# Kernel tuning notes

Hardware: AMD Instinct MI355X
Metric: run time of the kernel (lower is better)

The kernel has to match this reference:

```python
import jax, jax.numpy as jnp
import numpy as np
from jax import lax

DN = ('NCHW', 'OIHW', 'NCHW')


def conv_s2(x, w, b):
    # Conv2d(kernel=4, stride=2, padding=1): halves H,W
    y = lax.conv_general_dilated(x, w, (2, 2), ((1, 1), (1, 1)), dimension_numbers=DN)
    return y + b[None, :, None, None]


def conv_1x1(x, w, b):
    y = lax.conv_general_dilated(x, w, (1, 1), ((0, 0), (0, 0)), dimension_numbers=DN)
    return y + b[None, :, None, None]


def convT_s2(x, w, b):
    # torch ConvTranspose2d(kernel=4, stride=2, padding=1); torch weight layout [I,O,kh,kw]
    wt = jnp.flip(w, (2, 3)).transpose(1, 0, 2, 3)  # -> [O,I,kh,kw], spatially flipped
    y = lax.conv_general_dilated(x, wt, (1, 1), ((2, 2), (2, 2)),
                                 lhs_dilation=(2, 2), dimension_numbers=DN)
    return y + b[None, :, None, None]


def setup_inputs() -> dict:
    key = jax.random.key(0)
    ks = jax.random.split(key, 20)
    f32 = jnp.float32
    s = 0.05  # small init scale to keep activations sane
    inp = {
        'x': jax.random.uniform(ks[0], (32, 3, 256, 256), dtype=f32),
        # encoder
        'ew1': jax.random.normal(ks[1], (128, 3, 4, 4), f32) * s,
        'eb1': jnp.zeros((128,), f32),
        'ew2': jax.random.normal(ks[2], (256, 128, 4, 4), f32) * s,
        'eb2': jnp.zeros((256,), f32),
        'ew3': jax.random.normal(ks[3], (512, 256, 4, 4), f32) * s,
        'eb3': jnp.zeros((512,), f32),
        # pre-VQ 1x1 conv
        'pw': jax.random.normal(ks[4], (64, 512, 1, 1), f32) * s,
        'pb': jnp.zeros((64,), f32),
        # codebook (torch.randn in module)
        'emb': jax.random.normal(ks[5], (512, 64), f32),
        # decoder (ConvTranspose2d weights: [in, out, kh, kw])
        'dw1': jax.random.normal(ks[6], (64, 256, 4, 4), f32) * s,
        'db1': jnp.zeros((256,), f32),
        'dw2': jax.random.normal(ks[7], (256, 128, 4, 4), f32) * s,
        'db2': jnp.zeros((128,), f32),
        'dw3': jax.random.normal(ks[8], (128, 3, 4, 4), f32) * s,
        'db3': jnp.zeros((3,), f32),
    }
    return inp


def reference(x, ew1, eb1, ew2, eb2, ew3, eb3, pw, pb, emb,
              dw1, db1, dw2, db2, dw3, db3):
    # encoder
    h = jax.nn.relu(conv_s2(x, ew1, eb1))
    h = jax.nn.relu(conv_s2(h, ew2, eb2))
    h = jax.nn.relu(conv_s2(h, ew3, eb3))
    z_e = conv_1x1(h, pw, pb)  # [B, D, H, W]

    b, d, hh, ww = z_e.shape
    x_flat = z_e.reshape(b, d, hh * ww).transpose(0, 2, 1)  # [B, HW, D]
    # squared distances via expansion (same math, no [B,HW,K,D] blowup)
    x2 = jnp.sum(x_flat ** 2, axis=-1, keepdims=True)        # [B, HW, 1]
    e2 = jnp.sum(emb ** 2, axis=-1)                          # [K]
    dist = x2 - 2.0 * jnp.einsum('bnd,kd->bnk', x_flat, emb) + e2[None, None, :]
    indices = jnp.argmin(dist, axis=2)                       # [B, HW]
    zq_flat = emb[indices]                                   # [B, HW, D]
    z_q = zq_flat.transpose(0, 2, 1).reshape(b, d, hh, ww)

    quant_loss = (jnp.mean((zq_flat - x_flat) ** 2) * 2.0)   # matches detach-symmetric mse in fwd value

    # decoder
    y = jax.nn.relu(convT_s2(z_q, dw1, db1))
    y = jax.nn.relu(convT_s2(y, dw2, db2))
    y = jax.nn.sigmoid(convT_s2(y, dw3, db3))
    return (y, quant_loss)
```

## Files before the change

### kernel.cpp

```cpp
#include <hip/hip_runtime.h>
#include <cstddef>
#include <cstdint>

typedef __attribute__((ext_vector_type(8))) _Float16 half8;
typedef __attribute__((ext_vector_type(4))) float f32x4;

static __device__ __forceinline__ unsigned packhl(float v) {
  _Float16 h = (_Float16)v;
  _Float16 l = (_Float16)((v - (float)h) * 2048.0f);
  return (unsigned)__builtin_bit_cast(unsigned short, h) |
         ((unsigned)__builtin_bit_cast(unsigned short, l) << 16);
}


template<int CIN>
__global__ __launch_bounds__(256) void wsplit_k(
    const float* __restrict__ W, _Float16* __restrict__ Wh,
    _Float16* __restrict__ Wl, int Cout) {
  constexpr int NCB = CIN / 32;
  int idx = blockIdx.x * 256 + threadIdx.x;
  if (idx >= Cout * CIN) return;
  int ci = idx % CIN, co = idx / CIN;
  int cb = ci >> 5, k8 = (ci >> 3) & 3, j = ci & 7;
  const float* wp = W + (size_t)idx * 16;
#pragma unroll
  for (int tap = 0; tap < 16; ++tap) {
    float w = wp[tap];
    _Float16 wh = (_Float16)w;
    _Float16 wl = (_Float16)((w - (float)wh) * 2048.0f);
    size_t o = (((size_t)(tap * NCB + cb) * 4 + k8) * Cout + co) * 8 + j;
    Wh[o] = wh; Wl[o] = wl;
  }
}

template<int CIN>
__global__ __launch_bounds__(256) void wsplitT_k(
    const float* __restrict__ W, _Float16* __restrict__ Wh,
    _Float16* __restrict__ Wl, int Cout) {
  constexpr int NCB = CIN / 32;
  int idx = blockIdx.x * 256 + threadIdx.x;
  if (idx >= CIN * Cout) return;
  int co = idx % Cout, ci = idx / Cout;
  int cb = ci >> 5, k8 = (ci >> 3) & 3, j = ci & 7;
  const float* wp = W + (size_t)idx * 16;
#pragma unroll
  for (int t = 0; t < 16; ++t) {
    int py = (t >> 3) & 1, px = (t >> 2) & 1, i0 = (t >> 1) & 1, i1 = t & 1;
    int kh = py ? (i0 ? 2 : 0) : (i0 ? 3 : 1);
    int kw = px ? (i1 ? 2 : 0) : (i1 ? 3 : 1);
    float w = wp[kh * 4 + kw];
    _Float16 wh = (_Float16)w;
    _Float16 wl = (_Float16)((w - (float)wh) * 2048.0f);
    size_t o = (((size_t)(t * NCB + cb) * 4 + k8) * Cout + co) * 8 + j;
    Wh[o] = wh; Wl[o] = wl;
  }
}

__global__ __launch_bounds__(256) void border_k(
    char* base, int c8n, int H2, int W2, size_t SAI, size_t LOFF, int nimg) {
  int nb = 2 * W2 + 2 * (H2 - 2);
  int tot = nimg * c8n * 2 * nb;
  int idx = blockIdx.x * 256 + threadIdx.x;
  if (idx >= tot) return;
  int s = idx % nb; int r = idx / nb;
  int pl = r & 1; r >>= 1;
  int c8 = r % c8n; int b = r / c8n;
  int y, x;
  if (s < W2)            { y = 0;       x = s; }
  else if (s < 2 * W2)   { y = H2 - 1;  x = s - W2; }
  else { int t = s - 2 * W2; y = 1 + (t >> 1); x = (t & 1) ? W2 - 1 : 0; }
  size_t PLANE = (size_t)H2 * W2 * 16;
  char* p = base + (size_t)b * SAI + (size_t)pl * LOFF + (size_t)c8 * PLANE
            + ((size_t)y * W2 + x) * 16;
  *(uint4*)p = make_uint4(0, 0, 0, 0);
}

template<int CIN, int COUT, int CGRP, int NF, int RELU, int PACKOUT, int SPLITIN>
__global__ __launch_bounds__(256) void conv_mfma2(
    const void* __restrict__ inP, const _Float16* __restrict__ Whg,
    const _Float16* __restrict__ Wlg, const float* __restrict__ bias,
    float* __restrict__ out, int Hin, int Win, size_t inSAI, size_t inLOFF) {
  constexpr int NCB  = CIN / 32;
  constexpr int MT   = COUT / CGRP;
  constexpr int MF   = MT / 64;
  constexpr int ROWS = 2 * NF + 2;
  constexpr int NPOS = ROWS * 34;
  constexpr int K8S  = NPOS + 6;
  const int Hout = Hin >> 1, Wout = Win >> 1;
  const int TW = Wout >> 4;
  __shared__ half8 Bh[4 * K8S], Bl[4 * K8S];
  const int tid = threadIdx.x;
  const int lane = tid & 63, w = tid >> 6;
  const int l15 = lane & 15, k8 = lane >> 4;
  unsigned nwg = gridDim.x * gridDim.y;
  unsigned id  = blockIdx.y * gridDim.x + blockIdx.x;
  unsigned sw  = (id & 7) * (nwg >> 3) + (id >> 3);
  const int bx = sw % gridDim.x, by = sw / gridDim.x;
  const int tx = bx % TW, ty = bx / TW;
  const int cg = by % CGRP;
  const int b  = by / CGRP;
  const int oy0 = ty * NF, ox0 = tx << 4;
  const int iy_org = 2 * oy0 - 1, ix_org = 2 * ox0 - 1;
  const int cbase = cg * MT + w * (MT / 4);
  const size_t HW = (size_t)Hin * Win;
  const size_t tapStride = (size_t)NCB * 4 * COUT * 8;

  unsigned goff[4];
  const char* baseh = nullptr;
  size_t PLANE = 0;
  if (SPLITIN) {
    const int W2 = Win + 2;
    PLANE = (size_t)(Hin + 2) * W2 * 16;
    constexpr int S0[4] = {0, 64, 128, NPOS - 64};
#pragma unroll
    for (int t = 0; t < 4; ++t) {
      int s = S0[t] + lane;
      int r = s / 17, c = s - r * 17;
      int hy = r >> 1, p = r & 1;
      int hx = (c << 1) | p;
      int iy = iy_org + hy + 1, ix = ix_org + hx + 1;
      goff[t] = (unsigned)(((size_t)iy * W2 + ix) * 16);
    }
    baseh = (const char*)inP + ((size_t)b * inSAI) + (size_t)w * PLANE;
  }

  f32x4 accM[MF][NF], accX[MF][NF];
#pragma unroll
  for (int m = 0; m < MF; ++m)
#pragma unroll
    for (int nf = 0; nf < NF; ++nf) {
      accM[m][nf] = f32x4{0,0,0,0};
      accX[m][nf] = f32x4{0,0,0,0};
    }

  for (int cb = 0; cb < NCB; ++cb) {
    __syncthreads();
    if (SPLITIN) {
      const char* pc = baseh + (size_t)cb * 4 * PLANE;
      char* lh = (char*)&Bh[w * K8S];
      char* ll = (char*)&Bl[w * K8S];
      constexpr int S0[4] = {0, 64, 128, NPOS - 64};
#pragma unroll
      for (int t = 0; t < 4; ++t) {
        __builtin_amdgcn_global_load_lds(
            (const __attribute__((address_space(1))) void*)(pc + goff[t]),
            (__attribute__((address_space(3))) void*)(lh + S0[t] * 16), 16, 0, 0);
        __builtin_amdgcn_global_load_lds(
            (const __attribute__((address_space(1))) void*)(pc + inLOFF + goff[t]),
            (__attribute__((address_space(3))) void*)(ll + S0[t] * 16), 16, 0, 0);
      }
    } else {
      const unsigned* inU = (const unsigned*)inP;
      for (int u = tid; u < NPOS * 4; u += 256) {
        int kk = u / NPOS, pos = u - kk * NPOS;
        int hy = pos / 34, hx = pos - hy * 34;
        int iy = iy_org + hy, ix = ix_org + hx;
        bool ok = (unsigned)iy < (unsigned)Hin && (unsigned)ix < (unsigned)Win;
        uint4 qa = {0,0,0,0}, qb = {0,0,0,0};
        if (ok) {
          const uint4* gp = (const uint4*)(inU +
              (((size_t)b * (CIN / 8) + cb * 4 + kk) * HW + (size_t)iy * Win + ix) * 8);
          qa = gp[0]; qb = gp[1];
        }
        unsigned av[8] = {qa.x, qa.y, qa.z, qa.w, qb.x, qb.y, qb.z, qb.w};
        half8 vh, vl;
#pragma unroll
        for (int j = 0; j < 8; ++j) {
          vh[j] = __builtin_bit_cast(_Float16, (unsigned short)(av[j] & 0xffffu));
          vl[j] = __builtin_bit_cast(_Float16, (unsigned short)(av[j] >> 16));
        }
        int slotBase = (hy * 2 + (hx & 1)) * 17 + (hx >> 1);
        Bh[kk * K8S + slotBase] = vh;
        Bl[kk * K8S + slotBase] = vl;
      }
    }
    __syncthreads();
    const _Float16* aph = Whg + (((size_t)cb * 4 + k8) * COUT + cbase + l15) * 8;
    const _Float16* apl = Wlg + (((size_t)cb * 4 + k8) * COUT + cbase + l15) * 8;
    half8 ah[2][MF], al[2][MF];
#pragma unroll
    for (int m = 0; m < MF; ++m) {
      ah[0][m] = *(const half8*)(aph + m * 128);
      al[0][m] = *(const half8*)(apl + m * 128);
    }
#pragma unroll
    for (int tp = 0; tp < 16; ++tp) {
      const int cur = tp & 1, nxt = cur ^ 1;
      if (tp < 15) {
#pragma unroll
        for (int m = 0; m < MF; ++m) {
          ah[nxt][m] = *(const half8*)(aph + (size_t)(tp + 1) * tapStride + m * 128);
          al[nxt][m] = *(const half8*)(apl + (size_t)(tp + 1) * tapStride + m * 128);
        }
      }
      const int kh = tp >> 2, kw = tp & 3;
      const int p = kw & 1, cidx = kw >> 1;
#pragma unroll
      for (int nf = 0; nf < NF; ++nf) {
        const int slot = k8 * K8S + ((2 * nf + kh) * 2 + p) * 17 + l15 + cidx;
        const half8 bh = Bh[slot], bl = Bl[slot];
#pragma unroll
        for (int m = 0; m < MF; ++m) {
          accM[m][nf] = __builtin_amdgcn_mfma_f32_16x16x32_f16(ah[cur][m], bh, accM[m][nf], 0, 0, 0);
          accX[m][nf] = __builtin_amdgcn_mfma_f32_16x16x32_f16(ah[cur][m], bl, accX[m][nf], 0, 0, 0);
          accX[m][nf] = __builtin_amdgcn_mfma_f32_16x16x32_f16(al[cur][m], bh, accX[m][nf], 0, 0, 0);
        }
      }
    }
  }
#pragma unroll
  for (int m = 0; m < MF; ++m)
#pragma unroll
    for (int nf = 0; nf < NF; ++nf) {
      int oy = oy0 + nf, ox = ox0 + l15;
      if (PACKOUT) {
        unsigned pk[4];
#pragma unroll
        for (int i = 0; i < 4; ++i) {
          int co = cbase + m * 16 + k8 * 4 + i;
          float v = accM[m][nf][i] + accX[m][nf][i] * (1.0f / 2048.0f) + bias[co];
          if (RELU) v = fmaxf(v, 0.0f);
          pk[i] = packhl(v);
        }
        int co8 = (cbase + m * 16 + k8 * 4) >> 3;
        int j0 = (k8 & 1) * 4;
        unsigned* outU = (unsigned*)out;
        *(uint4*)(outU + (((size_t)b * (COUT / 8) + co8) * ((size_t)Hout * Wout)
                          + (size_t)oy * Wout + ox) * 8 + j0) =
            make_uint4(pk[0], pk[1], pk[2], pk[3]);
      } else {
#pragma unroll
        for (int i = 0; i < 4; ++i) {
          int co = cbase + m * 16 + k8 * 4 + i;
          float v = accM[m][nf][i] + accX[m][nf][i] * (1.0f / 2048.0f) + bias[co];
          if (RELU) v = fmaxf(v, 0.0f);
          out[(((size_t)b * COUT + co) * Hout + oy) * Wout + ox] = v;
        }
      }
    }
}

template<int CIN, int RELU, int PACKIN, int PACKOUT>
__global__ __launch_bounds__(256) void convT_mfma(
    const float* __restrict__ in, const _Float16* __restrict__ Whg,
    const _Float16* __restrict__ Wlg, const float* __restrict__ bias,
    float* __restrict__ out, int Cout, int Hin, int Win) {
  constexpr int NCB = CIN / 32;
  const int Hout = Hin * 2, Wout = Win * 2;
  const int TW = Win >> 4;
  __shared__ half8 Bh[4 * 72], Bl[4 * 72];
  const int tid = threadIdx.x;
  const int lane = tid & 63, w = tid >> 6;
  const int l15 = lane & 15, k8 = lane >> 4;
  const int tx = blockIdx.x % TW, ty = blockIdx.x / TW;
  const int cbo = blockIdx.y % (Cout >> 6);
  const int b   = blockIdx.y / (Cout >> 6);
  const int ty0 = ty << 1, tx0 = tx << 4;
  const int co0 = (cbo << 6) + (w << 4);
  const size_t HW = (size_t)Hin * Win;
  const size_t tapStride = (size_t)NCB * 4 * Cout * 8;

  f32x4 accM[4][2], accX[4][2];
#pragma unroll
  for (int p = 0; p < 4; ++p)
#pragma unroll
    for (int nf = 0; nf < 2; ++nf) {
      accM[p][nf] = f32x4{0,0,0,0};
      accX[p][nf] = f32x4{0,0,0,0};
    }

  for (int cb = 0; cb < NCB; ++cb) {
    __syncthreads();
    for (int u = tid; u < 288; u += 256) {
      int pos = u % 72, kk = u / 72;
      int r = pos / 18, c = pos - r * 18;
      int iy = ty0 - 1 + r, ix = tx0 - 1 + c;
      bool ok = (unsigned)iy < (unsigned)Hin && (unsigned)ix < (unsigned)Win;
      half8 vh, vl;
      if (PACKIN) {
        uint4 qa = {0,0,0,0}, qb = {0,0,0,0};
        if (ok) {
          const uint4* gp = (const uint4*)((const unsigned*)in +
              (((size_t)b * (CIN / 8) + cb * 4 + kk) * HW + (size_t)iy * Win + ix) * 8);
          qa = gp[0]; qb = gp[1];
        }
        unsigned av[8] = {qa.x, qa.y, qa.z, qa.w, qb.x, qb.y, qb.z, qb.w};
#pragma unroll
        for (int j = 0; j < 8; ++j) {
          vh[j] = __builtin_bit_cast(_Float16, (unsigned short)(av[j] & 0xffffu));
          vl[j] = __builtin_bit_cast(_Float16, (unsigned short)(av[j] >> 16));
        }
      } else {
        const float* gp = in + ((size_t)b * CIN + cb * 32 + kk * 8) * HW
                          + (ptrdiff_t)iy * Win + ix;
#pragma unroll
        for (int j = 0; j < 8; ++j) {
          float x = ok ? gp[(size_t)j * HW] : 0.0f;
          _Float16 xh = (_Float16)x;
          vh[j] = xh; vl[j] = (_Float16)((x - (float)xh) * 2048.0f);
        }
      }
      Bh[kk * 72 + pos] = vh;
      Bl[kk * 72 + pos] = vl;
    }
    __syncthreads();
    const _Float16* aph = Whg + (((size_t)cb * 4 + k8) * Cout + co0 + l15) * 8;
    const _Float16* apl = Wlg + (((size_t)cb * 4 + k8) * Cout + co0 + l15) * 8;
    half8 ahA = *(const half8*)(aph);
    half8 alA = *(const half8*)(apl);
#pragma unroll
    for (int t = 0; t < 16; ++t) {
      half8 ahN, alN;
      if (t < 15) {
        ahN = *(const half8*)(aph + (size_t)(t + 1) * tapStride);
        alN = *(const half8*)(apl + (size_t)(t + 1) * tapStride);
      }
      const int py = (t >> 3) & 1, px = (t >> 2) & 1;
      const int i0 = (t >> 1) & 1, i1 = t & 1;
      const int dy = py ? (i0 ? 0 : 1) : (i0 ? -1 : 0);
      const int dx = px ? (i1 ? 0 : 1) : (i1 ? -1 : 0);
      const int p = py * 2 + px;
#pragma unroll
      for (int nf = 0; nf < 2; ++nf) {
        int slot = k8 * 72 + (nf + 1 + dy) * 18 + (l15 + 1 + dx);
        half8 bh = Bh[slot], bl = Bl[slot];
        accM[p][nf] = __builtin_amdgcn_mfma_f32_16x16x32_f16(ahA, bh, accM[p][nf], 0, 0, 0);
        accX[p][nf] = __builtin_amdgcn_mfma_f32_16x16x32_f16(ahA, bl, accX[p][nf], 0, 0, 0);
        accX[p][nf] = __builtin_amdgcn_mfma_f32_16x16x32_f16(alA, bh, accX[p][nf], 0, 0, 0);
      }
      if (t < 15) { ahA = ahN; alA = alN; }
    }
  }
#pragma unroll
  for (int nf = 0; nf < 2; ++nf) {
#pragma unroll
    for (int i = 0; i < 4; ++i) {
      int co = co0 + k8 * 4 + i;
      float bb = bias[co];
#pragma unroll
      for (int py = 0; py < 2; ++py) {
        float v0 = accM[py * 2 + 0][nf][i] + accX[py * 2 + 0][nf][i] * (1.0f / 2048.0f) + bb;
        float v1 = accM[py * 2 + 1][nf][i] + accX[py * 2 + 1][nf][i] * (1.0f / 2048.0f) + bb;
        if (RELU) { v0 = fmaxf(v0, 0.0f); v1 = fmaxf(v1, 0.0f); }
        int oy = 2 * (ty0 + nf) + py, ox = 2 * (tx0 + l15);
        if (PACKOUT) {
          unsigned* outU = (unsigned*)out;
          int co8 = (co0 >> 3) + (k8 >> 1);
          int j = (k8 * 4 + i) & 7;
          size_t base = ((size_t)b * (Cout / 8) + co8) * ((size_t)Hout * Wout);
          outU[(base + (size_t)oy * Wout + ox) * 8 + j]     = packhl(v0);
          outU[(base + (size_t)oy * Wout + ox + 1) * 8 + j] = packhl(v1);
        } else {
          *(float2*)(out + (((size_t)b * Cout + co) * Hout + oy) * Wout + ox) =
              make_float2(v0, v1);
        }
      }
    }
  }
}


template<int CIN, int G, int RELU, int PACKOUT>
__global__ __launch_bounds__(256) void conv_t(
    const float* __restrict__ in, const float* __restrict__ wt,
    const float* __restrict__ bias, float* __restrict__ out,
    int Cout, int Hin, int Win, size_t oSAI, size_t oLOFF) {
  const int Hout = Hin >> 1, Wout = Win >> 1;
  const int TW = Wout >> 4;
  __shared__ float tile[34 * 35];
  int tid = threadIdx.x;
  int oxl = tid & 15, oyl = tid >> 4;
  int tyt = blockIdx.x / TW, txt = blockIdx.x - tyt * TW;
  int oy0 = tyt << 4, ox0 = txt << 4;
  int cg = blockIdx.y % (Cout / G);
  int b  = blockIdx.y / (Cout / G);
  int co0 = cg * G;
  const int iy_org = 2 * oy0 - 1, ix_org = 2 * ox0 - 1;
  const float* ip = in + (size_t)b * CIN * Hin * Win;
  float acc[G];
#pragma unroll
  for (int j = 0; j < G; ++j) acc[j] = bias[co0 + j];
  const int lbase = (2 * oyl) * 35 + 2 * oxl;
  for (int ci = 0; ci < CIN; ++ci) {
    const float* ic = ip + (size_t)ci * Hin * Win;
    __syncthreads();
#pragma unroll
    for (int k = 0; k < 5; ++k) {
      int idx = tid + k * 256;
      if (idx < 34 * 34) {
        int r = idx / 34, c = idx - r * 34;
        int iy = iy_org + r, ix = ix_org + c;
        float v = ((unsigned)iy < (unsigned)Hin && (unsigned)ix < (unsigned)Win)
                      ? ic[(size_t)iy * Win + ix] : 0.0f;
        tile[r * 35 + c] = v;
      }
    }
    __syncthreads();
    float xv[16];
#pragma unroll
    for (int kh = 0; kh < 4; ++kh)
#pragma unroll
      for (int kw = 0; kw < 4; ++kw)
        xv[kh * 4 + kw] = tile[lbase + kh * 35 + kw];
    const float* wc = wt + ((size_t)co0 * CIN + ci) * 16;
#pragma unroll
    for (int j = 0; j < G; ++j) {
      const float* wj = wc + (size_t)j * CIN * 16;
#pragma unroll
      for (int t2 = 0; t2 < 16; ++t2) acc[j] = fmaf(xv[t2], wj[t2], acc[j]);
    }
  }
  int oy = oy0 + oyl, ox = ox0 + oxl;
  if (RELU) {
#pragma unroll
    for (int j = 0; j < G; ++j) acc[j] = fmaxf(acc[j], 0.0f);
  }
  if (PACKOUT == 2) {
    const int W2 = Wout + 2;
    const size_t PLANE = (size_t)(Hout + 2) * W2 * 16;
    char* ob0 = (char*)out + (size_t)b * oSAI
                + ((size_t)(oy + 1) * W2 + ox + 1) * 16;
#pragma unroll
    for (int mb = 0; mb < G / 8; ++mb) {
      half8 hv, lv;
#pragma unroll
      for (int j = 0; j < 8; ++j) {
        float v = acc[mb * 8 + j];
        _Float16 h = (_Float16)v;
        hv[j] = h; lv[j] = (_Float16)((v - (float)h) * 2048.0f);
      }
      char* ob = ob0 + (size_t)((co0 >> 3) + mb) * PLANE;
      *(half8*)ob = hv;
      *(half8*)(ob + oLOFF) = lv;
    }
  } else {
    size_t cs = (size_t)Hout * Wout;
    float* op = out + ((size_t)(b * Cout + co0) * Hout + oy) * Wout + ox;
#pragma unroll
    for (int j = 0; j < G; ++j) op[(size_t)j * cs] = acc[j];
  }
}

template<int CIN, int G>
__global__ __launch_bounds__(256) void conv1x1_k(
    const float* __restrict__ in, const float* __restrict__ wt,
    const float* __restrict__ bias, float* __restrict__ out,
    int Cout, int HW) {
  int hw = blockIdx.x * 256 + threadIdx.x;
  int cg = blockIdx.y % (Cout / G);
  int b  = blockIdx.y / (Cout / G);
  int co0 = cg * G;
  const float* ip = in + (size_t)b * CIN * HW + hw;
  float acc[G];
#pragma unroll
  for (int j = 0; j < G; ++j) acc[j] = bias[co0 + j];
#pragma unroll 4
  for (int ci = 0; ci < CIN; ++ci) {
    float xv = ip[(size_t)ci * HW];
#pragma unroll
    for (int j = 0; j < G; ++j)
      acc[j] = fmaf(xv, wt[(size_t)(co0 + j) * CIN + ci], acc[j]);
  }
  float* op = out + ((size_t)(b * Cout + co0)) * HW + hw;
#pragma unroll
  for (int j = 0; j < G; ++j) op[(size_t)j * HW] = acc[j];
}

__global__ __launch_bounds__(128) void vq_k(
    const float* __restrict__ ze, const float* __restrict__ emb,
    float* __restrict__ zq, float* __restrict__ partial) {
  __shared__ float4 se4[128 * 16];
  __shared__ float red[128];
  int tid = threadIdx.x;
  int gid = blockIdx.x * 128 + tid;
  int b = gid >> 10, n = gid & 1023;
  const float* zp = ze + ((size_t)b << 16) + n;
  float4 v4[16];
#pragma unroll
  for (int d = 0; d < 16; ++d) {
    v4[d].x = zp[(size_t)(4 * d + 0) << 10];
    v4[d].y = zp[(size_t)(4 * d + 1) << 10];
    v4[d].z = zp[(size_t)(4 * d + 2) << 10];
    v4[d].w = zp[(size_t)(4 * d + 3) << 10];
  }
  float best = 1e30f; int bi = 0;
  for (int c = 0; c < 4; ++c) {
    __syncthreads();
    for (int i = tid; i < 2048; i += 128)
      se4[i] = ((const float4*)emb)[(c << 11) + i];
    __syncthreads();
    for (int k = 0; k < 128; ++k) {
      const float4* e = se4 + (k << 4);
      float s = 0.0f;
#pragma unroll
      for (int d = 0; d < 16; ++d) {
        float4 ev = e[d];
        float t0 = v4[d].x - ev.x; s = fmaf(t0, t0, s);
        float t1 = v4[d].y - ev.y; s = fmaf(t1, t1, s);
        float t2 = v4[d].z - ev.z; s = fmaf(t2, t2, s);
        float t3 = v4[d].w - ev.w; s = fmaf(t3, t3, s);
      }
      if (s < best) { best = s; bi = (c << 7) + k; }
    }
  }
  const float4* eb4 = (const float4*)emb + ((size_t)bi << 4);
  float* qp = zq + ((size_t)b << 16) + n;
  float ls = 0.0f;
#pragma unroll
  for (int d = 0; d < 16; ++d) {
    float4 q = eb4[d];
    qp[(size_t)(4 * d + 0) << 10] = q.x;
    qp[(size_t)(4 * d + 1) << 10] = q.y;
    qp[(size_t)(4 * d + 2) << 10] = q.z;
    qp[(size_t)(4 * d + 3) << 10] = q.w;
    float t0 = q.x - v4[d].x; ls = fmaf(t0, t0, ls);
    float t1 = q.y - v4[d].y; ls = fmaf(t1, t1, ls);
    float t2 = q.z - v4[d].z; ls = fmaf(t2, t2, ls);
    float t3 = q.w - v4[d].w; ls = fmaf(t3, t3, ls);
  }
  red[tid] = ls;
  __syncthreads();
  for (int s = 64; s > 0; s >>= 1) {
    if (tid < s) red[tid] += red[tid + s];
    __syncthreads();
  }
  if (tid == 0) partial[blockIdx.x] = red[0];
}

__global__ __launch_bounds__(256) void loss_fin(
    const float* __restrict__ partial, float* __restrict__ out) {
  __shared__ float red[256];
  int t = threadIdx.x;
  red[t] = partial[t];
  __syncthreads();
  for (int s = 128; s > 0; s >>= 1) {
    if (t < s) red[t] += red[t + s];
    __syncthreads();
  }
  if (t == 0) out[0] = red[0] * (2.0f / 2097152.0f);
}

template<int CIN, int G, int ACT>
__global__ __launch_bounds__(256) void convT_t(
    const float* __restrict__ in, const float* __restrict__ wt,
    const float* __restrict__ bias, float* __restrict__ out,
    int Cout, int Hin, int Win) {
  const int Hout = Hin * 2, Wout = Win * 2;
  const int TW = Win >> 4;
  __shared__ float tile[18 * 19];
  int tid = threadIdx.x;
  int txl = tid & 15, tyl = tid >> 4;
  int tyt = blockIdx.x / TW, txt = blockIdx.x - tyt * TW;
  int ty0 = tyt << 4, tx0 = txt << 4;
  int og = blockIdx.y % (Cout / G);
  int b  = blockIdx.y / (Cout / G);
  int o0 = og * G;
  const int iy_org = ty0 - 1, ix_org = tx0 - 1;
  const float* ip = in + (size_t)b * CIN * Hin * Win;
  float a00[G], a01[G], a10[G], a11[G];
#pragma unroll
  for (int j = 0; j < G; ++j) {
    float bb = bias[o0 + j];
    a00[j] = bb; a01[j] = bb; a10[j] = bb; a11[j] = bb;
  }
  const int lb = tyl * 19 + txl;
  for (int i = 0; i < CIN; ++i) {
    const float* ic = ip + (size_t)i * Hin * Win;
    __syncthreads();
#pragma unroll
    for (int k = 0; k < 2; ++k) {
      int idx = tid + k * 256;
      if (idx < 18 * 18) {
        int r = idx / 18, c = idx - r * 18;
        int iy = iy_org + r, ix = ix_org + c;
        float v = ((unsigned)iy < (unsigned)Hin && (unsigned)ix < (unsigned)Win)
                      ? ic[(size_t)iy * Win + ix] : 0.0f;
        tile[r * 19 + c] = v;
      }
    }
    __syncthreads();
    float x00 = tile[lb],          x01 = tile[lb + 1],      x02 = tile[lb + 2];
    float x10 = tile[lb + 19],     x11 = tile[lb + 20],     x12 = tile[lb + 21];
    float x20 = tile[lb + 38],     x21 = tile[lb + 39],     x22 = tile[lb + 40];
    const float* wv = wt + ((size_t)i * Cout + o0) * 16;
#pragma unroll
    for (int j = 0; j < G; ++j) {
      const float* w4 = wv + j * 16;
      a00[j] = fmaf(x11, w4[5],  fmaf(x10, w4[7],  fmaf(x01, w4[13], fmaf(x00, w4[15], a00[j]))));
      a01[j] = fmaf(x12, w4[4],  fmaf(x11, w4[6],  fmaf(x02, w4[12], fmaf(x01, w4[14], a01[j]))));
      a10[j] = fmaf(x21, w4[1],  fmaf(x20, w4[3],  fmaf(x11, w4[9],  fmaf(x10, w4[11], a10[j]))));
      a11[j] = fmaf(x22, w4[0],  fmaf(x21, w4[2],  fmaf(x12, w4[8],  fmaf(x11, w4[10], a11[j]))));
    }
  }
  size_t cs = (size_t)Hout * Wout;
  int ty = ty0 + tyl, tx = tx0 + txl;
  size_t base = ((size_t)(b * Cout + o0) * Hout + 2 * (size_t)ty) * Wout + 2 * tx;
#pragma unroll
  for (int j = 0; j < G; ++j) {
    float v00 = a00[j], v01 = a01[j], v10 = a10[j], v11 = a11[j];
    if (ACT == 1) {
      v00 = fmaxf(v00, 0.0f); v01 = fmaxf(v01, 0.0f);
      v10 = fmaxf(v10, 0.0f); v11 = fmaxf(v11, 0.0f);
    } else if (ACT == 2) {
      v00 = 1.0f / (1.0f + expf(-v00)); v01 = 1.0f / (1.0f + expf(-v01));
      v10 = 1.0f / (1.0f + expf(-v10)); v11 = 1.0f / (1.0f + expf(-v11));
    }
    *(float2*)(out + base + (size_t)j * cs)        = make_float2(v00, v01);
    *(float2*)(out + base + (size_t)j * cs + Wout) = make_float2(v10, v11);
  }
}

extern "C" void kernel_launch(void* const* d_in, const int* in_sizes, int n_in,
                              void* d_out, int out_size, void* d_ws, size_t ws_size,
                              hipStream_t stream) {
  const float* x   = (const float*)d_in[0];
  const float* ew1 = (const float*)d_in[1];
  const float* eb1 = (const float*)d_in[2];
  const float* ew2 = (const float*)d_in[3];
  const float* eb2 = (const float*)d_in[4];
  const float* ew3 = (const float*)d_in[5];
  const float* eb3 = (const float*)d_in[6];
  const float* pw  = (const float*)d_in[7];
  const float* pb  = (const float*)d_in[8];
  const float* emb = (const float*)d_in[9];
  const float* dw1 = (const float*)d_in[10];
  const float* db1 = (const float*)d_in[11];
  const float* dw2 = (const float*)d_in[12];
  const float* db2 = (const float*)d_in[13];
  const float* dw3 = (const float*)d_in[14];
  const float* db3 = (const float*)d_in[15];
  float* out = (float*)d_out;
  char* ws = (char*)d_ws;

  const size_t H1PLANE = 130ull * 130ull * 16ull;
  const size_t H1LOFF  = 16ull * H1PLANE;
  const size_t SAI     = 2ull * H1LOFF;
  const size_t PER  = SAI + 4194304ull + 2ull * 262144ull;
  const size_t WEXT = 4096ull + 13631488ull;
  int CB = 32;
  while (CB > 1 && (size_t)CB * PER + WEXT > ws_size) CB >>= 1;
  const size_t SA = (size_t)CB * SAI;
  const size_t SB = (size_t)CB * 4194304ull;
  const size_t SC = (size_t)CB * 262144ull;
  float* A    = (float*)(ws);
  float* Bp   = (float*)(ws + SA);
  float* ze   = (float*)(ws + SA + SB);
  float* zq   = (float*)(ws + SA + SB + SC);
  float* part = (float*)(ws + SA + SB + 2 * SC);
  _Float16* wh2  = (_Float16*)(ws + SA + SB + 2 * SC + 4096);
  _Float16* wl2  = wh2 + 524288;
  _Float16* wh3  = wl2 + 524288;
  _Float16* wl3  = wh3 + 2097152;
  _Float16* whT1 = wl3 + 2097152;
  _Float16* wlT1 = whT1 + 262144;
  _Float16* whT2 = wlT1 + 262144;
  _Float16* wlT2 = whT2 + 524288;

  wsplit_k<128><<<128, 256, 0, stream>>>(ew2, wh2, wl2, 256);
  wsplit_k<256><<<512, 256, 0, stream>>>(ew3, wh3, wl3, 512);
  wsplitT_k<64><<<64,  256, 0, stream>>>(dw1, whT1, wlT1, 256);
  wsplitT_k<256><<<128, 256, 0, stream>>>(dw2, whT2, wlT2, 128);

  for (int c0 = 0; c0 < 32; c0 += CB) {
    const float* xc = x + (size_t)c0 * 3 * 65536;
    float* outc = out + (size_t)c0 * 3 * 65536;
    {
      int nb = 2 * 130 + 2 * 128;
      int tot = CB * 16 * 2 * nb;
      border_k<<<(tot + 255) / 256, 256, 0, stream>>>(
          (char*)A, 16, 130, 130, SAI, H1LOFF, CB);
    }
    conv_t<3, 16, 1, 2><<<dim3(64, CB * 8), 256, 0, stream>>>(
        xc, ew1, eb1, A, 128, 256, 256, SAI, H1LOFF);
    conv_mfma2<128, 256, 1, 2, 1, 1, 1><<<dim3(128, CB), 256, 0, stream>>>(
        (const void*)A, wh2, wl2, eb2, Bp, 128, 128, SAI, H1LOFF);
    conv_mfma2<256, 512, 2, 2, 1, 0, 0><<<dim3(32, CB * 2), 256, 0, stream>>>(
        (const void*)Bp, wh3, wl3, eb3, A, 64, 64, 0, 0);
    conv1x1_k<512, 4><<<dim3(4, CB * 16), 256, 0, stream>>>(A, pw, pb, ze, 64, 1024);
    vq_k<<<CB * 8, 128, 0, stream>>>(ze, emb, zq, part + (size_t)c0 * 8);
    convT_mfma<64,  1, 0, 1><<<dim3(32,  CB * 4), 256, 0, stream>>>(zq, whT1, wlT1, db1, Bp, 256, 32, 32);
    convT_mfma<256, 1, 1, 0><<<dim3(128, CB * 2), 256, 0, stream>>>(Bp, whT2, wlT2, db2, A, 128, 64, 64);
    convT_t<128, 3, 2><<<dim3(64, CB * 1), 256, 0, stream>>>(A, dw3, db3, outc, 3, 128, 128);
  }
  loss_fin<<<1, 256, 0, stream>>>(part, out + (size_t)(out_size - 1));
}
```

Baseline: 2.352 ms.

## Generalize convT_mfma to multi-fragment output channels and add block swizzle

The transposed-conv MFMA kernel becomes templated on COUT and channel-group count, so each wave can own several 16-channel fragments. The second decoder layer now processes all 128 output channels in one block (MF=2), staging each input tile in LDS once instead of twice. Both convT launches also use a workgroup-id swizzle like the encoder kernels. The cost is twice the accumulator registers in the second decoder layer, which may reduce occupancy. An unused XMAP template parameter is added to conv_mfma2.

```diff
diff --git a/kernel.cpp b/kernel.cpp
--- a/kernel.cpp
+++ b/kernel.cpp
@@ -75,7 +75,8 @@
   *(uint4*)p = make_uint4(0, 0, 0, 0);
 }
 
-template<int CIN, int COUT, int CGRP, int NF, int RELU, int PACKOUT, int SPLITIN>
+template<int CIN, int COUT, int CGRP, int NF, int RELU, int PACKOUT, int SPLITIN,
+         int XMAP>
 __global__ __launch_bounds__(256) void conv_mfma2(
     const void* __restrict__ inP, const _Float16* __restrict__ Whg,
     const _Float16* __restrict__ Wlg, const float* __restrict__ bias,
@@ -92,13 +93,16 @@
   const int tid = threadIdx.x;
   const int lane = tid & 63, w = tid >> 6;
   const int l15 = lane & 15, k8 = lane >> 4;
-  unsigned nwg = gridDim.x * gridDim.y;
-  unsigned id  = blockIdx.y * gridDim.x + blockIdx.x;
-  unsigned sw  = (id & 7) * (nwg >> 3) + (id >> 3);
-  const int bx = sw % gridDim.x, by = sw / gridDim.x;
-  const int tx = bx % TW, ty = bx / TW;
-  const int cg = by % CGRP;
-  const int b  = by / CGRP;
+  int tx, ty, cg, b;
+  {
+    unsigned nwg = gridDim.x * gridDim.y;
+    unsigned id  = blockIdx.y * gridDim.x + blockIdx.x;
+    unsigned sw  = (id & 7) * (nwg >> 3) + (id >> 3);
+    const int bx = sw % gridDim.x, by = sw / gridDim.x;
+    tx = bx % TW; ty = bx / TW;
+    cg = by % CGRP;
+    b  = by / CGRP;
+  }
   const int oy0 = ty * NF, ox0 = tx << 4;
   const int iy_org = 2 * oy0 - 1, ix_org = 2 * ox0 - 1;
   const int cbase = cg * MT + w * (MT / 4);
@@ -240,34 +244,45 @@
     }
 }
 
-template<int CIN, int RELU, int PACKIN, int PACKOUT>
+template<int CIN, int COUT, int CGRP, int RELU, int PACKIN, int PACKOUT, int SWZ>
 __global__ __launch_bounds__(256) void convT_mfma(
     const float* __restrict__ in, const _Float16* __restrict__ Whg,
     const _Float16* __restrict__ Wlg, const float* __restrict__ bias,
-    float* __restrict__ out, int Cout, int Hin, int Win) {
+    float* __restrict__ out, int Hin, int Win) {
   constexpr int NCB = CIN / 32;
+  constexpr int MT  = COUT / CGRP;
+  constexpr int MF  = MT / 64;
   const int Hout = Hin * 2, Wout = Win * 2;
   const int TW = Win >> 4;
   __shared__ half8 Bh[4 * 72], Bl[4 * 72];
   const int tid = threadIdx.x;
   const int lane = tid & 63, w = tid >> 6;
   const int l15 = lane & 15, k8 = lane >> 4;
-  const int tx = blockIdx.x % TW, ty = blockIdx.x / TW;
-  const int cbo = blockIdx.y % (Cout >> 6);
-  const int b   = blockIdx.y / (Cout >> 6);
+  int bx = blockIdx.x, by = blockIdx.y;
+  if (SWZ) {
+    unsigned nwg = gridDim.x * gridDim.y;
+    unsigned id  = (unsigned)by * gridDim.x + bx;
+    unsigned sw  = (id & 7) * (nwg >> 3) + (id >> 3);
+    bx = (int)(sw % gridDim.x); by = (int)(sw / gridDim.x);
+  }
+  const int tx = bx % TW, ty = bx / TW;
+  const int cg = by % CGRP;
+  const int b  = by / CGRP;
   const int ty0 = ty << 1, tx0 = tx << 4;
-  const int co0 = (cbo << 6) + (w << 4);
+  const int cbase = cg * MT + w * (MT / 4);
   const size_t HW = (size_t)Hin * Win;
-  const size_t tapStride = (size_t)NCB * 4 * Cout * 8;
-
-  f32x4 accM[4][2], accX[4][2];
-#pragma unroll
-  for (int p = 0; p < 4; ++p)
-#pragma unroll
-    for (int nf = 0; nf < 2; ++nf) {
-      accM[p][nf] = f32x4{0,0,0,0};
-      accX[p][nf] = f32x4{0,0,0,0};
-    }
+  const size_t tapStride = (size_t)NCB * 4 * COUT * 8;
+
+  f32x4 accM[MF][4][2], accX[MF][4][2];
+#pragma unroll
+  for (int m = 0; m < MF; ++m)
+#pragma unroll
+    for (int p = 0; p < 4; ++p)
+#pragma unroll
+      for (int nf = 0; nf < 2; ++nf) {
+        accM[m][p][nf] = f32x4{0,0,0,0};
+        accX[m][p][nf] = f32x4{0,0,0,0};
+      }
 
   for (int cb = 0; cb < NCB; ++cb) {
     __syncthreads();
@@ -304,16 +319,23 @@
       Bl[kk * 72 + pos] = vl;
     }
     __syncthreads();
-    const _Float16* aph = Whg + (((size_t)cb * 4 + k8) * Cout + co0 + l15) * 8;
-    const _Float16* apl = Wlg + (((size_t)cb * 4 + k8) * Cout + co0 + l15) * 8;
-    half8 ahA = *(const half8*)(aph);
-    half8 alA = *(const half8*)(apl);
+    const _Float16* aph = Whg + (((size_t)cb * 4 + k8) * COUT + cbase + l15) * 8;
+    const _Float16* apl = Wlg + (((size_t)cb * 4 + k8) * COUT + cbase + l15) * 8;
+    half8 ah[2][MF], al[2][MF];
+#pragma unroll
+    for (int m = 0; m < MF; ++m) {
+      ah[0][m] = *(const half8*)(aph + m * 128);
+      al[0][m] = *(const half8*)(apl + m * 128);
+    }
 #pragma unroll
     for (int t = 0; t < 16; ++t) {
-      half8 ahN, alN;
+      const int cur = t & 1, nxt = cur ^ 1;
       if (t < 15) {
-        ahN = *(const half8*)(aph + (size_t)(t + 1) * tapStride);
-        alN = *(const half8*)(apl + (size_t)(t + 1) * tapStride);
+#pragma unroll
+        for (int m = 0; m < MF; ++m) {
+          ah[nxt][m] = *(const half8*)(aph + (size_t)(t + 1) * tapStride + m * 128);
+          al[nxt][m] = *(const half8*)(apl + (size_t)(t + 1) * tapStride + m * 128);
+        }
       }
       const int py = (t >> 3) & 1, px = (t >> 2) & 1;
       const int i0 = (t >> 1) & 1, i1 = t & 1;
@@ -324,35 +346,41 @@
       for (int nf = 0; nf < 2; ++nf) {
         int slot = k8 * 72 + (nf + 1 + dy) * 18 + (l15 + 1 + dx);
         half8 bh = Bh[slot], bl = Bl[slot];
-        accM[p][nf] = __builtin_amdgcn_mfma_f32_16x16x32_f16(ahA, bh, accM[p][nf], 0, 0, 0);
-        accX[p][nf] = __builtin_amdgcn_mfma_f32_16x16x32_f16(ahA, bl, accX[p][nf], 0, 0, 0);
-        accX[p][nf] = __builtin_amdgcn_mfma_f32_16x16x32_f16(alA, bh, accX[p][nf], 0, 0, 0);
-      }
-      if (t < 15) { ahA = ahN; alA = alN; }
-    }
-  }
-#pragma unroll
-  for (int nf = 0; nf < 2; ++nf) {
-#pragma unroll
-    for (int i = 0; i < 4; ++i) {
-      int co = co0 + k8 * 4 + i;
-      float bb = bias[co];
-#pragma unroll
-      for (int py = 0; py < 2; ++py) {
-        float v0 = accM[py * 2 + 0][nf][i] + accX[py * 2 + 0][nf][i] * (1.0f / 2048.0f) + bb;
-        float v1 = accM[py * 2 + 1][nf][i] + accX[py * 2 + 1][nf][i] * (1.0f / 2048.0f) + bb;
-        if (RELU) { v0 = fmaxf(v0, 0.0f); v1 = fmaxf(v1, 0.0f); }
-        int oy = 2 * (ty0 + nf) + py, ox = 2 * (tx0 + l15);
-        if (PACKOUT) {
-          unsigned* outU = (unsigned*)out;
-          int co8 = (co0 >> 3) + (k8 >> 1);
-          int j = (k8 * 4 + i) & 7;
-          size_t base = ((size_t)b * (Cout / 8) + co8) * ((size_t)Hout * Wout);
-          outU[(base + (size_t)oy * Wout + ox) * 8 + j]     = packhl(v0);
-          outU[(base + (size_t)oy * Wout + ox + 1) * 8 + j] = packhl(v1);
-        } else {
-          *(float2*)(out + (((size_t)b * Cout + co) * Hout + oy) * Wout + ox) =
-              make_float2(v0, v1);
+#pragma unroll
+        for (int m = 0; m < MF; ++m) {
+          accM[m][p][nf] = __builtin_amdgcn_mfma_f32_16x16x32_f16(ah[cur][m], bh, accM[m][p][nf], 0, 0, 0);
+          accX[m][p][nf] = __builtin_amdgcn_mfma_f32_16x16x32_f16(ah[cur][m], bl, accX[m][p][nf], 0, 0, 0);
+          accX[m][p][nf] = __builtin_amdgcn_mfma_f32_16x16x32_f16(al[cur][m], bh, accX[m][p][nf], 0, 0, 0);
+        }
+      }
+    }
+  }
+#pragma unroll
+  for (int m = 0; m < MF; ++m) {
+    const int co0m = cbase + m * 16;
+#pragma unroll
+    for (int nf = 0; nf < 2; ++nf) {
+#pragma unroll
+      for (int i = 0; i < 4; ++i) {
+        int co = co0m + k8 * 4 + i;
+        float bb = bias[co];
+#pragma unroll
+        for (int py = 0; py < 2; ++py) {
+          float v0 = accM[m][py * 2 + 0][nf][i] + accX[m][py * 2 + 0][nf][i] * (1.0f / 2048.0f) + bb;
+          float v1 = accM[m][py * 2 + 1][nf][i] + accX[m][py * 2 + 1][nf][i] * (1.0f / 2048.0f) + bb;
+          if (RELU) { v0 = fmaxf(v0, 0.0f); v1 = fmaxf(v1, 0.0f); }
+          int oy = 2 * (ty0 + nf) + py, ox = 2 * (tx0 + l15);
+          if (PACKOUT) {
+            unsigned* outU = (unsigned*)out;
+            int co8 = (co0m >> 3) + (k8 >> 1);
+            int j = (k8 * 4 + i) & 7;
+            size_t base = ((size_t)b * (COUT / 8) + co8) * ((size_t)Hout * Wout);
+            outU[(base + (size_t)oy * Wout + ox) * 8 + j]     = packhl(v0);
+            outU[(base + (size_t)oy * Wout + ox + 1) * 8 + j] = packhl(v1);
+          } else {
+            *(float2*)(out + (((size_t)b * COUT + co) * Hout + oy) * Wout + ox) =
+                make_float2(v0, v1);
+          }
         }
       }
     }
@@ -672,14 +700,16 @@
     }
     conv_t<3, 16, 1, 2><<<dim3(64, CB * 8), 256, 0, stream>>>(
         xc, ew1, eb1, A, 128, 256, 256, SAI, H1LOFF);
-    conv_mfma2<128, 256, 1, 2, 1, 1, 1><<<dim3(128, CB), 256, 0, stream>>>(
+    conv_mfma2<128, 256, 1, 2, 1, 1, 1, 0><<<dim3(128, CB), 256, 0, stream>>>(
         (const void*)A, wh2, wl2, eb2, Bp, 128, 128, SAI, H1LOFF);
-    conv_mfma2<256, 512, 2, 2, 1, 0, 0><<<dim3(32, CB * 2), 256, 0, stream>>>(
+    conv_mfma2<256, 512, 2, 2, 1, 0, 0, 0><<<dim3(32, CB * 2), 256, 0, stream>>>(
         (const void*)Bp, wh3, wl3, eb3, A, 64, 64, 0, 0);
     conv1x1_k<512, 4><<<dim3(4, CB * 16), 256, 0, stream>>>(A, pw, pb, ze, 64, 1024);
     vq_k<<<CB * 8, 128, 0, stream>>>(ze, emb, zq, part + (size_t)c0 * 8);
-    convT_mfma<64,  1, 0, 1><<<dim3(32,  CB * 4), 256, 0, stream>>>(zq, whT1, wlT1, db1, Bp, 256, 32, 32);
-    convT_mfma<256, 1, 1, 0><<<dim3(128, CB * 2), 256, 0, stream>>>(Bp, whT2, wlT2, db2, A, 128, 64, 64);
+    convT_mfma<64, 256, 4, 1, 0, 1, 1><<<dim3(32, CB * 4), 256, 0, stream>>>(
+        zq, whT1, wlT1, db1, Bp, 32, 32);
+    convT_mfma<256, 128, 1, 1, 1, 0, 1><<<dim3(128, CB), 256, 0, stream>>>(
+        Bp, whT2, wlT2, db2, A, 64, 64);
     convT_t<128, 3, 2><<<dim3(64, CB * 1), 256, 0, stream>>>(A, dw3, db3, outc, 3, 128, 128);
   }
   loss_fin<<<1, 256, 0, stream>>>(part, out + (size_t)(out_size - 1));
```

Result: slower. 2.514 ms (+6.9%).
